# Optimization experiments

Measured on AMD Instinct MI355X. Metric: run time of the kernel, lower is better.

The kernel has to match this reference:

```python
import jax, jax.numpy as jnp
import numpy as np

N = 100000   # nodes
E = 1600000  # edges (before self-loops)
IN, HID, OUT = 128, 128, 64


def setup_inputs() -> dict:
    key = jax.random.key(0)
    ks = jax.random.split(key, 10)
    x = jax.random.normal(ks[0], (N, IN), dtype=jnp.float32)
    edge_index = jax.random.randint(ks[1], (2, E), 0, N)
    edge_weight = jax.random.uniform(ks[2], (E,), dtype=jnp.float32)
    # glorot-style init for the three GCNConv linear layers (with bias, PyG default)
    W1 = jax.random.normal(ks[3], (IN, HID), dtype=jnp.float32) * (1.0 / np.sqrt(IN))
    b1 = jnp.zeros((HID,), dtype=jnp.float32)
    W2 = jax.random.normal(ks[4], (HID, HID), dtype=jnp.float32) * (1.0 / np.sqrt(HID))
    b2 = jnp.zeros((HID,), dtype=jnp.float32)
    W3 = jax.random.normal(ks[5], (HID, OUT), dtype=jnp.float32) * (1.0 / np.sqrt(HID))
    b3 = jnp.zeros((OUT,), dtype=jnp.float32)
    return {"x": x, "edge_index": edge_index, "edge_weight": edge_weight,
            "W1": W1, "b1": b1, "W2": W2, "b2": b2, "W3": W3, "b3": b3}


def _gcn_norm(edge_index, edge_weight, num_nodes):
    """Add self-loops (weight 1) and compute symmetric D^-1/2 A D^-1/2 norm."""
    loop = jnp.arange(num_nodes)
    row = jnp.concatenate([edge_index[0], loop])
    col = jnp.concatenate([edge_index[1], loop])
    ew = jnp.concatenate([edge_weight, jnp.ones((num_nodes,), edge_weight.dtype)])
    deg = jax.ops.segment_sum(ew, col, num_segments=num_nodes)
    dinv = jnp.where(deg > 0, jax.lax.rsqrt(jnp.where(deg > 0, deg, 1.0)), 0.0)
    norm = dinv[row] * ew * dinv[col]  # [E+N]
    return row, col, norm


def _gcn_conv(h, row, col, norm, W, b, num_nodes):
    h = h @ W                                   # [N, d_out] dense transform first
    msg = h[row] * norm[:, None]                # gather + scale  [E+N, d_out]
    out = jax.ops.segment_sum(msg, col, num_segments=num_nodes)  # scatter-add
    return out + b


def reference(x, edge_index, edge_weight, W1, b1, W2, b2, W3, b3):
    num_nodes = x.shape[0]
    row, col, norm = _gcn_norm(edge_index, edge_weight, num_nodes)
    h = jax.nn.relu(_gcn_conv(x, row, col, norm, W1, b1, num_nodes))
    # dropout is identity in eval mode
    h = jax.nn.relu(_gcn_conv(h, row, col, norm, W2, b2, num_nodes))
    return _gcn_conv(h, row, col, norm, W3, b3, num_nodes)
```

## Files before the change

### kernel.cpp

```cpp
#include <hip/hip_runtime.h>
#include <hip/hip_bf16.h>
#include <hip/hip_fp16.h>


#define K_DIM 128
#define EPB 4096

using h4 = __attribute__((ext_vector_type(4))) _Float16;
using h8 = __attribute__((ext_vector_type(8))) _Float16;
using f16x4 = h4;
using f16x8 = h8;
typedef float f32x4 __attribute__((ext_vector_type(4)));

__global__ __launch_bounds__(256) void mhist_kernel(const int* __restrict__ col,
                                                    int* __restrict__ Hm, int e, int nb) {
    __shared__ int lcnt[1024];
    int blk = blockIdx.x, t = threadIdx.x;
    for (int i = t; i < nb; i += 256) lcnt[i] = 0;
    __syncthreads();
    int base = blk * EPB, end = min(base + EPB, e);
    for (int i = base + t; i < end; i += 256) atomicAdd(&lcnt[col[i] >> 7], 1);
    __syncthreads();
    for (int i = t; i < nb; i += 256) Hm[(size_t)blk * nb + i] = lcnt[i];
}

__global__ __launch_bounds__(256) void colscan_kernel(int* __restrict__ Hm,
                                                      int* __restrict__ bcnt,
                                                      int nblk, int nb) {
    int t = blockIdx.x * 4 + (threadIdx.x >> 6);
    int lane = threadIdx.x & 63;
    if (t >= nb) return;
    int carry = 0;
    for (int c0 = 0; c0 < nblk; c0 += 64) {
        int b = c0 + lane;
        int x = (b < nblk) ? Hm[(size_t)b * nb + t] : 0;
        int v = x;
        #pragma unroll
        for (int d = 1; d < 64; d <<= 1) {
            int y = __shfl_up(v, d, 64);
            if (lane >= d) v += y;
        }
        if (b < nblk) Hm[(size_t)b * nb + t] = carry + v - x;
        carry += __shfl(v, 63, 64);
    }
    if (lane == 0) bcnt[t] = carry;
}

__global__ __launch_bounds__(1024) void bscan2_kernel(const int* __restrict__ bcnt,
                                                      int* __restrict__ bptr,
                                                      int* __restrict__ nodeptr,
                                                      int nb, int nN, int etot) {
    __shared__ int wsum[16];
    int t = threadIdx.x, lane = t & 63, wid = t >> 6;
    int x = (t < nb) ? bcnt[t] : 0;
    int v = x;
    #pragma unroll
    for (int d = 1; d < 64; d <<= 1) {
        int y = __shfl_up(v, d, 64);
        if (lane >= d) v += y;
    }
    if (lane == 63) wsum[wid] = v;
    __syncthreads();
    if (wid == 0) {
        int s = (lane < 16) ? wsum[lane] : 0;
        #pragma unroll
        for (int d = 1; d < 16; d <<= 1) {
            int y = __shfl_up(s, d, 64);
            if (lane >= d) s += y;
        }
        if (lane < 16) wsum[lane] = s;
    }
    __syncthreads();
    int woff = (wid > 0) ? wsum[wid - 1] : 0;
    if (t < nb) bptr[t] = v + woff - x;
    if (t == 0) { bptr[nb] = etot; nodeptr[nN] = etot; }
}

__global__ void addbase_kernel(int* __restrict__ Hm, const int* __restrict__ bptr,
                               int nblk, int nb) {
    int i = blockIdx.x * blockDim.x + threadIdx.x;
    if (i < nblk * nb) Hm[i] += bptr[i % nb];
}

__global__ __launch_bounds__(256) void mscatter_kernel(const int* __restrict__ row,
                                                       const int* __restrict__ col,
                                                       const float* __restrict__ ew,
                                                       const int* __restrict__ Hm,
                                                       int2* __restrict__ ebuf,
                                                       int e, int nb) {
    __shared__ int2 sbuf[EPB];
    __shared__ unsigned short sbkt[EPB];
    __shared__ int lcnt[1024], lbase[1024], lfill[1024], garr[1024];
    int blk = blockIdx.x, t = threadIdx.x, lane = t & 63, wid = t >> 6;
    int base = blk * EPB, end = min(base + EPB, e);
    int cnt = end - base;
    if (cnt <= 0) return;
    for (int i = t; i < nb; i += 256) { garr[i] = Hm[(size_t)blk * nb + i]; lcnt[i] = 0; }
    __syncthreads();
    for (int i = base + t; i < end; i += 256) atomicAdd(&lcnt[col[i] >> 7], 1);
    __syncthreads();
    if (wid == 0) {
        int carry = 0;
        for (int c0 = 0; c0 < nb; c0 += 64) {
            int idx = c0 + lane;
            int x = (idx < nb) ? lcnt[idx] : 0;
            int v = x;
            #pragma unroll
            for (int d = 1; d < 64; d <<= 1) {
                int y = __shfl_up(v, d, 64);
                if (lane >= d) v += y;
            }
            if (idx < nb) { lbase[idx] = carry + v - x; lfill[idx] = carry + v - x; }
            carry += __shfl(v, 63, 64);
        }
    }
    __syncthreads();
    for (int i = base + t; i < end; i += 256) {
        int c = col[i];
        int b = c >> 7;
        int p = atomicAdd(&lfill[b], 1);
        sbuf[p] = make_int2(row[i] | ((c & 127) << 20), __float_as_int(ew[i]));
        sbkt[p] = (unsigned short)b;
    }
    __syncthreads();
    for (int j = t; j < cnt; j += 256) {
        int b = sbkt[j];
        ebuf[garr[b] + (j - lbase[b])] = sbuf[j];
    }
}

__global__ __launch_bounds__(256) void bbuild_kernel(const int2* __restrict__ ebuf,
                                                     const int* __restrict__ bptr,
                                                     int2* __restrict__ csr,
                                                     int* __restrict__ ptr, int n) {
    __shared__ int cnt[128];
    __shared__ int fil[128];
    int b = blockIdx.x;
    int t = threadIdx.x;
    int s = bptr[b], e = bptr[b + 1];
    if (t < 128) cnt[t] = 0;
    __syncthreads();
    for (int k = s + t; k < e; k += 256) {
        int c = (ebuf[k].x >> 20) & 127;
        atomicAdd(&cnt[c], 1);
    }
    __syncthreads();
    if (t < 64) {
        int lane = t;
        int v0 = cnt[lane], v1 = cnt[lane + 64];
        int i0 = v0, i1 = v1;
        #pragma unroll
        for (int d = 1; d < 64; d <<= 1) {
            int y0 = __shfl_up(i0, d, 64);
            int y1 = __shfl_up(i1, d, 64);
            if (lane >= d) { i0 += y0; i1 += y1; }
        }
        int tot0 = __shfl(i0, 63, 64);
        int e0 = i0 - v0;
        int e1 = i1 - v1 + tot0;
        fil[lane] = e0; fil[lane + 64] = e1;
        int node0 = b * 128 + lane;
        int node1 = node0 + 64;
        if (node0 < n) ptr[node0] = s + e0;
        if (node1 < n) ptr[node1] = s + e1;
    }
    __syncthreads();
    for (int k = s + t; k < e; k += 256) {
        int2 v = ebuf[k];
        int c = (v.x >> 20) & 127;
        int p = atomicAdd(&fil[c], 1);
        csr[s + p] = make_int2(v.x & 0xFFFFF, v.y);
    }
}

__global__ __launch_bounds__(256) void sortdeg_kernel(int2* __restrict__ csr,
                                                      const int* __restrict__ ptr,
                                                      float* __restrict__ dinv, int n) {
    int node = blockIdx.x * 4 + (threadIdx.x >> 6);
    int lane = threadIdx.x & 63;
    if (node >= n) return;
    int s = ptr[node], e = ptr[node + 1];
    int len = e - s;
    if (len <= 64) {
        int mx = 0x7FFFFFFF;
        unsigned my = 0xFFFFFFFFu;
        if (lane < len) {
            int2 v = csr[s + lane];
            mx = v.x; my = (unsigned)v.y;
        }
        #pragma unroll
        for (int k = 2; k <= 64; k <<= 1) {
            #pragma unroll
            for (int j = k >> 1; j > 0; j >>= 1) {
                int ox = __shfl_xor(mx, j, 64);
                unsigned oy = (unsigned)__shfl_xor((int)my, j, 64);
                bool up = ((lane & k) == 0);
                bool lower = ((lane & j) == 0);
                bool keep_min = (up == lower);
                bool me_gt  = (mx > ox) || (mx == ox && my > oy);
                bool oth_gt = (ox > mx) || (ox == mx && oy > my);
                bool take = keep_min ? me_gt : oth_gt;
                if (take) { mx = ox; my = oy; }
            }
        }
        if (lane < len) csr[s + lane] = make_int2(mx, (int)my);
        float w = (lane < len) ? __uint_as_float(my) : 0.f;
        #pragma unroll
        for (int d = 32; d; d >>= 1) w += __shfl_xor(w, d, 64);
        if (lane == 0) dinv[node] = rsqrtf(1.0f + w);
    } else {
        if (lane == 0) {
            for (int k = s + 1; k < e; ++k) {
                int2 key = csr[k];
                int j = k - 1;
                while (j >= s) {
                    int2 cj = csr[j];
                    bool gt = (cj.x > key.x) ||
                              (cj.x == key.x && (unsigned)cj.y > (unsigned)key.y);
                    if (!gt) break;
                    csr[j + 1] = cj;
                    --j;
                }
                csr[j + 1] = key;
            }
            float sum = 1.0f;
            for (int k = s; k < e; ++k) sum += __int_as_float(csr[k].y);
            dinv[node] = rsqrtf(sum);
        }
    }
}

__global__ void wcast_kernel(const float* __restrict__ W, _Float16* __restrict__ Wt,
                             int douts) {
    int i = blockIdx.x * blockDim.x + threadIdx.x;
    if (i < 128 * douts) {
        int k = i / douts, c = i % douts;
        Wt[c * 128 + k] = (_Float16)W[i];
    }
}

template <int DOUT, bool FP16IN>
__global__ __launch_bounds__(256) void mgemm_kernel(const void* __restrict__ Ap,
                                                    const _Float16* __restrict__ Wt,
                                                    const float* __restrict__ dinv,
                                                    _Float16* __restrict__ Tout, int nrows) {
    constexpr int BM = 128;
    constexpr int NCB = DOUT / 16;
    __shared__ f16x8 Als[BM * 16];
    __shared__ f16x8 Wls[DOUT * 16];
    int t = threadIdx.x;
    int row0 = blockIdx.x * BM;

    const f16x8* Wt8 = (const f16x8*)Wt;
    for (int i = t; i < DOUT * 16; i += 256) {
        int r = i >> 4, s = i & 15;
        Wls[r * 16 + (s ^ (r & 7))] = Wt8[i];
    }
    if constexpr (FP16IN) {
        const f16x8* A8 = (const f16x8*)Ap;
        for (int i = t; i < BM * 16; i += 256) {
            int r = i >> 4, s = i & 15;
            f16x8 v = {};
            int gr = row0 + r;
            if (gr < nrows) v = A8[(size_t)gr * 16 + s];
            Als[r * 16 + (s ^ (r & 7))] = v;
        }
    } else {
        const float* A = (const float*)Ap;
        f16x4* Als4 = (f16x4*)Als;
        for (int i = t; i < BM * 32; i += 256) {
            int r = i >> 5, c4 = i & 31;
            float4 v = make_float4(0.f, 0.f, 0.f, 0.f);
            int gr = row0 + r;
            if (gr < nrows) v = ((const float4*)(A + (size_t)gr * 128))[c4];
            f16x4 h;
            h[0] = (_Float16)v.x; h[1] = (_Float16)v.y;
            h[2] = (_Float16)v.z; h[3] = (_Float16)v.w;
            Als4[r * 32 + (c4 ^ ((r & 7) << 1))] = h;
        }
    }
    __syncthreads();

    int w = t >> 6, l = t & 63;
    int lcol = l & 15, lk = l >> 4;
    int wr0 = w * 32;

    f16x8 af[2][4];
    #pragma unroll
    for (int rb = 0; rb < 2; ++rb) {
        int r = wr0 + rb * 16 + lcol;
        #pragma unroll
        for (int kc = 0; kc < 4; ++kc) {
            int s = kc * 4 + lk;
            af[rb][kc] = Als[r * 16 + (s ^ (r & 7))];
        }
    }

    f32x4 acc[2][NCB] = {};
    #pragma unroll
    for (int cb = 0; cb < NCB; ++cb) {
        int c = cb * 16 + lcol;
        f16x8 bf[4];
        #pragma unroll
        for (int kc = 0; kc < 4; ++kc) {
            int s = kc * 4 + lk;
            bf[kc] = Wls[c * 16 + (s ^ (c & 7))];
        }
        #pragma unroll
        for (int rb = 0; rb < 2; ++rb) {
            #pragma unroll
            for (int kc = 0; kc < 4; ++kc)
                acc[rb][cb] = __builtin_amdgcn_mfma_f32_16x16x32_f16(
                    af[rb][kc], bf[kc], acc[rb][cb], 0, 0, 0);
        }
    }

    #pragma unroll
    for (int rb = 0; rb < 2; ++rb) {
        #pragma unroll
        for (int reg = 0; reg < 4; ++reg) {
            int gr = row0 + wr0 + rb * 16 + lk * 4 + reg;
            if (gr >= nrows) continue;
            float di = dinv[gr];
            #pragma unroll
            for (int cb = 0; cb < NCB; ++cb) {
                int c = cb * 16 + lcol;
                Tout[(size_t)gr * DOUT + c] = (_Float16)(acc[rb][cb][reg] * di);
            }
        }
    }
}

__global__ __launch_bounds__(256) void agg128_kernel(const _Float16* __restrict__ T,
                                                     const int* __restrict__ ptr,
                                                     const int2* __restrict__ csr,
                                                     const float* __restrict__ dinv,
                                                     const float* __restrict__ bias,
                                                     _Float16* __restrict__ out, int n) {
    int node = blockIdx.x * 16 + (threadIdx.x >> 4);
    int g = threadIdx.x & 15;
    if (node >= n) return;
    int s = ptr[node], e = ptr[node + 1];
    float di = dinv[node];
    const h8* Tv = (const h8*)T;
    float acc[8] = {};
    int k = s;
    for (; k + 3 < e; k += 4) {
        int2 e0 = csr[k], e1 = csr[k + 1], e2 = csr[k + 2], e3 = csr[k + 3];
        h8 v0 = Tv[(size_t)e0.x * 16 + g];
        h8 v1 = Tv[(size_t)e1.x * 16 + g];
        h8 v2 = Tv[(size_t)e2.x * 16 + g];
        h8 v3 = Tv[(size_t)e3.x * 16 + g];
        float w0 = __int_as_float(e0.y), w1 = __int_as_float(e1.y);
        float w2 = __int_as_float(e2.y), w3 = __int_as_float(e3.y);
        #pragma unroll
        for (int j = 0; j < 8; ++j) acc[j] += w0 * (float)v0[j];
        #pragma unroll
        for (int j = 0; j < 8; ++j) acc[j] += w1 * (float)v1[j];
        #pragma unroll
        for (int j = 0; j < 8; ++j) acc[j] += w2 * (float)v2[j];
        #pragma unroll
        for (int j = 0; j < 8; ++j) acc[j] += w3 * (float)v3[j];
    }
    for (; k < e; ++k) {
        int2 e0 = csr[k];
        h8 v0 = Tv[(size_t)e0.x * 16 + g];
        float w0 = __int_as_float(e0.y);
        #pragma unroll
        for (int j = 0; j < 8; ++j) acc[j] += w0 * (float)v0[j];
    }
    h8 hs = Tv[(size_t)node * 16 + g];
    #pragma unroll
    for (int j = 0; j < 8; ++j) acc[j] += (float)hs[j];
    float4 b0 = ((const float4*)bias)[g * 2];
    float4 b1 = ((const float4*)bias)[g * 2 + 1];
    float bb[8] = {b0.x, b0.y, b0.z, b0.w, b1.x, b1.y, b1.z, b1.w};
    h8 o;
    #pragma unroll
    for (int j = 0; j < 8; ++j) {
        float v = di * acc[j] + bb[j];
        o[j] = (_Float16)fmaxf(v, 0.f);
    }
    ((h8*)out)[(size_t)node * 16 + g] = o;
}

__global__ __launch_bounds__(256) void agg64_kernel(const _Float16* __restrict__ T,
                                                    const int* __restrict__ ptr,
                                                    const int2* __restrict__ csr,
                                                    const float* __restrict__ dinv,
                                                    const float* __restrict__ bias,
                                                    float* __restrict__ out, int n) {
    int node = blockIdx.x * 32 + (threadIdx.x >> 3);
    int g = threadIdx.x & 7;
    if (node >= n) return;
    int s = ptr[node], e = ptr[node + 1];
    float di = dinv[node];
    const h8* Tv = (const h8*)T;
    float acc[8] = {};
    int k = s;
    for (; k + 3 < e; k += 4) {
        int2 e0 = csr[k], e1 = csr[k + 1], e2 = csr[k + 2], e3 = csr[k + 3];
        h8 v0 = Tv[(size_t)e0.x * 8 + g];
        h8 v1 = Tv[(size_t)e1.x * 8 + g];
        h8 v2 = Tv[(size_t)e2.x * 8 + g];
        h8 v3 = Tv[(size_t)e3.x * 8 + g];
        float w0 = __int_as_float(e0.y), w1 = __int_as_float(e1.y);
        float w2 = __int_as_float(e2.y), w3 = __int_as_float(e3.y);
        #pragma unroll
        for (int j = 0; j < 8; ++j) acc[j] += w0 * (float)v0[j];
        #pragma unroll
        for (int j = 0; j < 8; ++j) acc[j] += w1 * (float)v1[j];
        #pragma unroll
        for (int j = 0; j < 8; ++j) acc[j] += w2 * (float)v2[j];
        #pragma unroll
        for (int j = 0; j < 8; ++j) acc[j] += w3 * (float)v3[j];
    }
    for (; k < e; ++k) {
        int2 e0 = csr[k];
        h8 v0 = Tv[(size_t)e0.x * 8 + g];
        float w0 = __int_as_float(e0.y);
        #pragma unroll
        for (int j = 0; j < 8; ++j) acc[j] += w0 * (float)v0[j];
    }
    h8 hs = Tv[(size_t)node * 8 + g];
    #pragma unroll
    for (int j = 0; j < 8; ++j) acc[j] += (float)hs[j];
    float4 b0 = ((const float4*)bias)[g * 2];
    float4 b1 = ((const float4*)bias)[g * 2 + 1];
    float4 o0, o1;
    o0.x = di * acc[0] + b0.x; o0.y = di * acc[1] + b0.y;
    o0.z = di * acc[2] + b0.z; o0.w = di * acc[3] + b0.w;
    o1.x = di * acc[4] + b1.x; o1.y = di * acc[5] + b1.y;
    o1.z = di * acc[6] + b1.z; o1.w = di * acc[7] + b1.w;
    ((float4*)out)[(size_t)node * 16 + g * 2] = o0;
    ((float4*)out)[(size_t)node * 16 + g * 2 + 1] = o1;
}

extern "C" void kernel_launch(void* const* d_in, const int* in_sizes, int n_in,
                              void* d_out, int out_size, void* d_ws, size_t ws_size,
                              hipStream_t stream) {
    const float* x   = (const float*)d_in[0];
    const int* eidx  = (const int*)d_in[1];
    const float* ew  = (const float*)d_in[2];
    const float* W1  = (const float*)d_in[3];
    const float* b1  = (const float*)d_in[4];
    const float* W2  = (const float*)d_in[5];
    const float* b2  = (const float*)d_in[6];
    const float* W3  = (const float*)d_in[7];
    const float* b3  = (const float*)d_in[8];

    const int N = in_sizes[0] / K_DIM;
    const int E = in_sizes[2];
    const int* erow = eidx;
    const int* ecol = eidx + E;
    const int NB = (N + 127) / 128;
    const int NBLK = (E + EPB - 1) / EPB;

    size_t off = 0;
    auto carve = [&](size_t bytes) {
        char* p = (char*)d_ws + off;
        off += (bytes + 255) & ~(size_t)255;
        return (void*)p;
    };
    int*   Hm   = (int*)carve((size_t)NBLK * NB * 4);
    int*   bcnt = (int*)carve((size_t)NB * 4);
    int*   bptr = (int*)carve((size_t)(NB + 1) * 4);
    int*   ptr  = (int*)carve((size_t)(N + 1) * 4);
    float* dinv = (float*)carve((size_t)N * 4);
    int2*  csr  = (int2*)carve((size_t)E * 8);
    size_t ubytes = (size_t)E * 8;
    if ((size_t)N * 128 * 2 > ubytes) ubytes = (size_t)N * 128 * 2;
    void* uni = carve(ubytes);
    int2*     ebuf = (int2*)uni;
    _Float16* Tf   = (_Float16*)uni;
    _Float16* Hact = (_Float16*)carve((size_t)N * 128 * 2);
    _Float16* T3   = (_Float16*)carve((size_t)N * 64 * 2);
    _Float16* Wt1 = (_Float16*)carve(128 * 128 * 2);
    _Float16* Wt2 = (_Float16*)carve(128 * 128 * 2);
    _Float16* Wt3 = (_Float16*)carve(64 * 128 * 2);
    (void)ws_size;

    float* out = (float*)d_out;

    wcast_kernel<<<64, 256, 0, stream>>>(W1, Wt1, 128);
    wcast_kernel<<<64, 256, 0, stream>>>(W2, Wt2, 128);
    wcast_kernel<<<32, 256, 0, stream>>>(W3, Wt3, 64);

    mhist_kernel<<<NBLK, 256, 0, stream>>>(ecol, Hm, E, NB);
    colscan_kernel<<<(NB + 3) / 4, 256, 0, stream>>>(Hm, bcnt, NBLK, NB);
    bscan2_kernel<<<1, 1024, 0, stream>>>(bcnt, bptr, ptr, NB, N, E);
    addbase_kernel<<<(NBLK * NB + 255) / 256, 256, 0, stream>>>(Hm, bptr, NBLK, NB);
    mscatter_kernel<<<NBLK, 256, 0, stream>>>(erow, ecol, ew, Hm, ebuf, E, NB);
    bbuild_kernel<<<NB, 256, 0, stream>>>(ebuf, bptr, csr, ptr, N);
    sortdeg_kernel<<<(N + 3) / 4, 256, 0, stream>>>(csr, ptr, dinv, N);

    int gG = (N + 127) / 128;
    int gAgg16 = (N + 15) / 16;
    int gAgg32 = (N + 31) / 32;

    mgemm_kernel<128, false><<<gG, 256, 0, stream>>>(x, Wt1, dinv, Tf, N);
    agg128_kernel<<<gAgg16, 256, 0, stream>>>(Tf, ptr, csr, dinv, b1, Hact, N);
    mgemm_kernel<128, true><<<gG, 256, 0, stream>>>(Hact, Wt2, dinv, Tf, N);
    agg128_kernel<<<gAgg16, 256, 0, stream>>>(Tf, ptr, csr, dinv, b2, Hact, N);
    mgemm_kernel<64, true><<<gG, 256, 0, stream>>>(Hact, Wt3, dinv, T3, N);
    agg64_kernel<<<gAgg32, 256, 0, stream>>>(T3, ptr, csr, dinv, b3, out, N);
}
```

Before: 332.9 us.

## Widen CSR buckets to 256 nodes, fold base-add into scatter, merge weight casts

Bucket size for the two-level counting sort goes from 128 to 256 destination nodes, which halves the number of buckets and so shrinks the per-block histogram matrix, the column scan work and the shared-memory arrays. The separate addbase pass is removed; mscatter now adds the bucket base offset when it loads its per-block offsets. The three weight-cast launches are merged into one kernel. Together these cut kernel launches and preprocessing traffic, but each bbuild block now sorts twice as many edges, so that kernel runs with fewer, heavier blocks.

```diff
diff --git a/kernel.cpp b/kernel.cpp
--- a/kernel.cpp
+++ b/kernel.cpp
@@ -5,6 +5,8 @@
 
 #define K_DIM 128
 #define EPB 4096
+#define BSH 8
+#define NBMAX 512
 
 using h4 = __attribute__((ext_vector_type(4))) _Float16;
 using h8 = __attribute__((ext_vector_type(8))) _Float16;
@@ -14,12 +16,12 @@
 
 __global__ __launch_bounds__(256) void mhist_kernel(const int* __restrict__ col,
                                                     int* __restrict__ Hm, int e, int nb) {
-    __shared__ int lcnt[1024];
+    __shared__ int lcnt[NBMAX];
     int blk = blockIdx.x, t = threadIdx.x;
     for (int i = t; i < nb; i += 256) lcnt[i] = 0;
     __syncthreads();
     int base = blk * EPB, end = min(base + EPB, e);
-    for (int i = base + t; i < end; i += 256) atomicAdd(&lcnt[col[i] >> 7], 1);
+    for (int i = base + t; i < end; i += 256) atomicAdd(&lcnt[col[i] >> BSH], 1);
     __syncthreads();
     for (int i = t; i < nb; i += 256) Hm[(size_t)blk * nb + i] = lcnt[i];
 }
@@ -76,28 +78,26 @@
     if (t == 0) { bptr[nb] = etot; nodeptr[nN] = etot; }
 }
 
-__global__ void addbase_kernel(int* __restrict__ Hm, const int* __restrict__ bptr,
-                               int nblk, int nb) {
-    int i = blockIdx.x * blockDim.x + threadIdx.x;
-    if (i < nblk * nb) Hm[i] += bptr[i % nb];
-}
-
 __global__ __launch_bounds__(256) void mscatter_kernel(const int* __restrict__ row,
                                                        const int* __restrict__ col,
                                                        const float* __restrict__ ew,
                                                        const int* __restrict__ Hm,
+                                                       const int* __restrict__ bptr,
                                                        int2* __restrict__ ebuf,
                                                        int e, int nb) {
     __shared__ int2 sbuf[EPB];
     __shared__ unsigned short sbkt[EPB];
-    __shared__ int lcnt[1024], lbase[1024], lfill[1024], garr[1024];
+    __shared__ int lcnt[NBMAX], lbase[NBMAX], lfill[NBMAX], garr[NBMAX];
     int blk = blockIdx.x, t = threadIdx.x, lane = t & 63, wid = t >> 6;
     int base = blk * EPB, end = min(base + EPB, e);
     int cnt = end - base;
     if (cnt <= 0) return;
-    for (int i = t; i < nb; i += 256) { garr[i] = Hm[(size_t)blk * nb + i]; lcnt[i] = 0; }
-    __syncthreads();
-    for (int i = base + t; i < end; i += 256) atomicAdd(&lcnt[col[i] >> 7], 1);
+    for (int i = t; i < nb; i += 256) {
+        garr[i] = Hm[(size_t)blk * nb + i] + bptr[i];
+        lcnt[i] = 0;
+    }
+    __syncthreads();
+    for (int i = base + t; i < end; i += 256) atomicAdd(&lcnt[col[i] >> BSH], 1);
     __syncthreads();
     if (wid == 0) {
         int carry = 0;
@@ -117,9 +117,9 @@
     __syncthreads();
     for (int i = base + t; i < end; i += 256) {
         int c = col[i];
-        int b = c >> 7;
+        int b = c >> BSH;
         int p = atomicAdd(&lfill[b], 1);
-        sbuf[p] = make_int2(row[i] | ((c & 127) << 20), __float_as_int(ew[i]));
+        sbuf[p] = make_int2(row[i] | ((c & 255) << 20), __float_as_int(ew[i]));
         sbkt[p] = (unsigned short)b;
     }
     __syncthreads();
@@ -133,43 +133,36 @@
                                                      const int* __restrict__ bptr,
                                                      int2* __restrict__ csr,
                                                      int* __restrict__ ptr, int n) {
-    __shared__ int cnt[128];
-    __shared__ int fil[128];
-    int b = blockIdx.x;
-    int t = threadIdx.x;
+    __shared__ int cnt[256];
+    __shared__ int fil[256];
+    __shared__ int wtot[4];
+    int b = blockIdx.x, t = threadIdx.x, lane = t & 63, wid = t >> 6;
     int s = bptr[b], e = bptr[b + 1];
-    if (t < 128) cnt[t] = 0;
+    cnt[t] = 0;
+    __syncthreads();
+    for (int k = s + t; k < e; k += 256) atomicAdd(&cnt[(ebuf[k].x >> 20) & 255], 1);
+    __syncthreads();
+    int x = cnt[t];
+    int v = x;
+    #pragma unroll
+    for (int d = 1; d < 64; d <<= 1) {
+        int y = __shfl_up(v, d, 64);
+        if (lane >= d) v += y;
+    }
+    if (lane == 63) wtot[wid] = v;
+    __syncthreads();
+    int woff = 0;
+    for (int j = 0; j < wid; ++j) woff += wtot[j];
+    int excl = woff + v - x;
+    fil[t] = excl;
+    int node = b * 256 + t;
+    if (node < n) ptr[node] = s + excl;
     __syncthreads();
     for (int k = s + t; k < e; k += 256) {
-        int c = (ebuf[k].x >> 20) & 127;
-        atomicAdd(&cnt[c], 1);
-    }
-    __syncthreads();
-    if (t < 64) {
-        int lane = t;
-        int v0 = cnt[lane], v1 = cnt[lane + 64];
-        int i0 = v0, i1 = v1;
-        #pragma unroll
-        for (int d = 1; d < 64; d <<= 1) {
-            int y0 = __shfl_up(i0, d, 64);
-            int y1 = __shfl_up(i1, d, 64);
-            if (lane >= d) { i0 += y0; i1 += y1; }
-        }
-        int tot0 = __shfl(i0, 63, 64);
-        int e0 = i0 - v0;
-        int e1 = i1 - v1 + tot0;
-        fil[lane] = e0; fil[lane + 64] = e1;
-        int node0 = b * 128 + lane;
-        int node1 = node0 + 64;
-        if (node0 < n) ptr[node0] = s + e0;
-        if (node1 < n) ptr[node1] = s + e1;
-    }
-    __syncthreads();
-    for (int k = s + t; k < e; k += 256) {
-        int2 v = ebuf[k];
-        int c = (v.x >> 20) & 127;
+        int2 vv = ebuf[k];
+        int c = (vv.x >> 20) & 255;
         int p = atomicAdd(&fil[c], 1);
-        csr[s + p] = make_int2(v.x & 0xFFFFF, v.y);
+        csr[s + p] = make_int2(vv.x & 0xFFFFF, vv.y);
     }
 }
 
@@ -230,12 +223,22 @@
     }
 }
 
-__global__ void wcast_kernel(const float* __restrict__ W, _Float16* __restrict__ Wt,
-                             int douts) {
-    int i = blockIdx.x * blockDim.x + threadIdx.x;
-    if (i < 128 * douts) {
-        int k = i / douts, c = i % douts;
-        Wt[c * 128 + k] = (_Float16)W[i];
+__global__ __launch_bounds__(256) void wcast3_kernel(const float* __restrict__ W1,
+                                                     const float* __restrict__ W2,
+                                                     const float* __restrict__ W3,
+                                                     _Float16* __restrict__ Wt1,
+                                                     _Float16* __restrict__ Wt2,
+                                                     _Float16* __restrict__ Wt3) {
+    int i = blockIdx.x * 256 + threadIdx.x;
+    if (i < 16384) {
+        int k = i / 128, c = i % 128;
+        Wt1[c * 128 + k] = (_Float16)W1[i];
+    } else if (i < 32768) {
+        int j = i - 16384, k = j / 128, c = j % 128;
+        Wt2[c * 128 + k] = (_Float16)W2[j];
+    } else if (i < 40960) {
+        int j = i - 32768, k = j / 64, c = j % 64;
+        Wt3[c * 128 + k] = (_Float16)W3[j];
     }
 }
 
@@ -453,7 +456,7 @@
     const int E = in_sizes[2];
     const int* erow = eidx;
     const int* ecol = eidx + E;
-    const int NB = (N + 127) / 128;
+    const int NB = (N + 255) / 256;
     const int NBLK = (E + EPB - 1) / EPB;
 
     size_t off = 0;
@@ -482,15 +485,12 @@
 
     float* out = (float*)d_out;
 
-    wcast_kernel<<<64, 256, 0, stream>>>(W1, Wt1, 128);
-    wcast_kernel<<<64, 256, 0, stream>>>(W2, Wt2, 128);
-    wcast_kernel<<<32, 256, 0, stream>>>(W3, Wt3, 64);
+    wcast3_kernel<<<160, 256, 0, stream>>>(W1, W2, W3, Wt1, Wt2, Wt3);
 
     mhist_kernel<<<NBLK, 256, 0, stream>>>(ecol, Hm, E, NB);
     colscan_kernel<<<(NB + 3) / 4, 256, 0, stream>>>(Hm, bcnt, NBLK, NB);
     bscan2_kernel<<<1, 1024, 0, stream>>>(bcnt, bptr, ptr, NB, N, E);
-    addbase_kernel<<<(NBLK * NB + 255) / 256, 256, 0, stream>>>(Hm, bptr, NBLK, NB);
-    mscatter_kernel<<<NBLK, 256, 0, stream>>>(erow, ecol, ew, Hm, ebuf, E, NB);
+    mscatter_kernel<<<NBLK, 256, 0, stream>>>(erow, ecol, ew, Hm, bptr, ebuf, E, NB);
     bbuild_kernel<<<NB, 256, 0, stream>>>(ebuf, bptr, csr, ptr, N);
     sortdeg_kernel<<<(N + 3) / 4, 256, 0, stream>>>(csr, ptr, dinv, N);
 
```

New measurement: 326.6 us. No clear change (-1.9%).
